# Optimization experiments

Hardware: AMD Instinct MI355X
Metric: run time of the kernel (lower is better)

The kernel has to match this reference:

```python
import jax, jax.numpy as jnp
import numpy as np

NEG_SLOPE = 0.2  # PyG GATConv default negative_slope


def setup_inputs() -> dict:
    key = jax.random.key(0)
    ks = jax.random.split(key, 5)
    N, E, F_in, F_out = 50000, 800000, 100, 200
    x = jax.random.normal(ks[0], (N, F_in), dtype=jnp.float32)
    edge_index = jax.random.randint(ks[1], (2, E), 0, N, dtype=jnp.int32)
    W = jax.random.normal(ks[2], (F_in, F_out), dtype=jnp.float32) / np.float32(np.sqrt(F_in))
    att_src = jax.random.normal(ks[3], (F_out,), dtype=jnp.float32) * 0.1
    att_dst = jax.random.normal(ks[4], (F_out,), dtype=jnp.float32) * 0.1
    bias = jnp.zeros((F_out,), dtype=jnp.float32)
    return {"x": x, "edge_index": edge_index, "W": W,
            "att_src": att_src, "att_dst": att_dst, "bias": bias}


def reference(x, edge_index, W, att_src, att_dst, bias):
    # GATConv (heads=1, concat=True, add_self_loops=True) followed by mean over nodes.
    N = x.shape[0]
    h = x @ W                                   # [N, F_out] transformed node features
    loops = jnp.arange(N, dtype=edge_index.dtype)
    src = jnp.concatenate([edge_index[0], loops])  # [E+N] source node per edge
    dst = jnp.concatenate([edge_index[1], loops])  # [E+N] destination node per edge
    # per-node attention logits
    a_s = h @ att_src                           # [N]
    a_d = h @ att_dst                           # [N]
    e = jax.nn.leaky_relu(a_s[src] + a_d[dst], NEG_SLOPE)  # [E+N]
    # numerically stable softmax over incoming edges of each destination node
    m = jax.ops.segment_max(e, dst, num_segments=N)        # [N]
    ex = jnp.exp(e - m[dst])                                # [E+N]
    denom = jax.ops.segment_sum(ex, dst, num_segments=N)    # [N]
    alpha = ex / denom[dst]                                  # [E+N]
    # scatter-add weighted messages
    out = jax.ops.segment_sum(alpha[:, None] * h[src], dst, num_segments=N) + bias  # [N, F_out]
    return jnp.mean(out, axis=0, keepdims=True)  # [1, F_out]
```

## Files before the change

### kernel.cpp

```cpp
#include <hip/hip_runtime.h>

#define NEG_SLOPE 0.2f
#define NBLK 256
#define RSH  6
#define RBIN 64
#define CAP  1536
#define MAXB 1024
#define CSB  256

typedef unsigned int uint;


__global__ void k_f1(const float* __restrict__ W, const float* __restrict__ att_src,
                     const float* __restrict__ att_dst, const int* __restrict__ ei,
                     float* __restrict__ wsv, float* __restrict__ wdv,
                     uint* __restrict__ cntA, uint* __restrict__ cntB,
                     uint* __restrict__ recA, uint* __restrict__ recB,
                     int E, int N, int B, int F_out) {
    __shared__ uint hA[MAXB], hB[MAXB];
    __shared__ float l_as[256], l_ad[256];
    int tid = threadIdx.x;
    int blk = blockIdx.x;
    if (blk == 0) {
        if (tid < 200) { l_as[tid] = att_src[tid]; l_ad[tid] = att_dst[tid]; }
        __syncthreads();
        if (tid < 200) {
            int k = tid >> 1, j = tid & 1;
            const float* row = W + (size_t)k * F_out + j * 100;
            const float* as = l_as + j * 100;
            const float* ad = l_ad + j * 100;
            float s0 = 0.f, s1 = 0.f;
            #pragma unroll
            for (int i = 0; i < 100; ++i) {
                float w = row[i];
                s0 = fmaf(w, as[i], s0);
                s1 = fmaf(w, ad[i], s1);
            }
            s0 += __shfl_xor(s0, 1);
            s1 += __shfl_xor(s1, 1);
            if (j == 0) { wsv[k] = s0; wdv[k] = s1; }
        }
    } else if (blk <= NBLK) {
        int hb = blk - 1;
        for (int b = tid; b < B; b += 256) { hA[b] = 0u; hB[b] = 0u; }
        __syncthreads();
        if ((E & 3) == 0) {
            int stride = NBLK * 256 * 4;
            for (int i = (hb * 256 + tid) * 4; i < E; i += stride) {
                int4 s4 = *reinterpret_cast<const int4*>(ei + i);
                int4 d4 = *reinterpret_cast<const int4*>(ei + E + i);
                atomicAdd(&hA[d4.x >> RSH], 1u); atomicAdd(&hB[s4.x >> RSH], 1u);
                atomicAdd(&hA[d4.y >> RSH], 1u); atomicAdd(&hB[s4.y >> RSH], 1u);
                atomicAdd(&hA[d4.z >> RSH], 1u); atomicAdd(&hB[s4.z >> RSH], 1u);
                atomicAdd(&hA[d4.w >> RSH], 1u); atomicAdd(&hB[s4.w >> RSH], 1u);
            }
        } else {
            int stride = NBLK * 256;
            for (int i = hb * 256 + tid; i < E; i += stride) {
                int s = ei[i], d = ei[E + i];
                atomicAdd(&hA[d >> RSH], 1u); atomicAdd(&hB[s >> RSH], 1u);
            }
        }
        __syncthreads();
        for (int b = tid; b < B; b += 256) {
            cntA[(size_t)hb * B + b] = hA[b];
            cntB[(size_t)hb * B + b] = hB[b];
        }
    } else {
        int idx = blk - NBLK - 1;
        int n0 = idx * 512;
        int n1 = min(N, n0 + 512);
        for (int n = n0 + tid; n < n1; n += 256) {
            int b = n >> RSH, l = n & (RBIN - 1);
            uint rec = ((uint)l << 16) | (uint)n;
            size_t slot = (size_t)b * CAP + l;
            recA[slot] = rec;
            recB[slot] = rec;
        }
    }
}

__global__ void k_f2(const float* __restrict__ x, const float* __restrict__ wsv,
                     const float* __restrict__ wdv, float* __restrict__ a_s,
                     float* __restrict__ a_d, uint* __restrict__ cntA,
                     uint* __restrict__ cntB, uint* __restrict__ totA,
                     uint* __restrict__ totB, int N, int B, int NODEB) {
    __shared__ float lws[100], lwd[100];
    __shared__ float p0[256], p1[256];
    __shared__ uint sv[NBLK];
    int tid = threadIdx.x;
    int blk = blockIdx.x;
    if (blk < NODEB) {
        if (tid < 100) { lws[tid] = wsv[tid]; lwd[tid] = wdv[tid]; }
        __syncthreads();
        int r = tid / 25, q = tid - r * 25;
        int row = blk * 10 + r;
        float s0 = 0.f, s1 = 0.f;
        if (tid < 250 && row < N) {
            float4 v = *reinterpret_cast<const float4*>(x + (size_t)row * 100 + q * 4);
            const float* ws = lws + q * 4;
            const float* wd = lwd + q * 4;
            s0 = v.x * ws[0] + v.y * ws[1] + v.z * ws[2] + v.w * ws[3];
            s1 = v.x * wd[0] + v.y * wd[1] + v.z * wd[2] + v.w * wd[3];
        }
        p0[tid] = s0;
        p1[tid] = s1;
        __syncthreads();
        if (tid < 20) {
            int rr = tid >> 1;
            int row2 = blk * 10 + rr;
            if (row2 < N) {
                const float* p = (tid & 1) ? p1 : p0;
                float acc = 0.f;
                #pragma unroll
                for (int j = 0; j < 25; ++j) acc += p[rr * 25 + j];
                if (tid & 1) a_d[row2] = acc;
                else         a_s[row2] = acc;
            }
        }
    } else {
        int bi = blk - NODEB;
        int isB = bi >= B;
        int b = isB ? bi - B : bi;
        uint* cnt = isB ? cntB : cntA;
        uint* tot = isB ? totB : totA;
        int sc = N - b * RBIN; if (sc > RBIN) sc = RBIN;
        uint v = cnt[(size_t)tid * B + b];
        sv[tid] = v;
        __syncthreads();
        #pragma unroll
        for (int off = 1; off < NBLK; off <<= 1) {
            uint y = (tid >= off) ? sv[tid - off] : 0u;
            __syncthreads();
            sv[tid] += y;
            __syncthreads();
        }
        uint incl = sv[tid];
        cnt[(size_t)tid * B + b] = (uint)b * CAP + (uint)sc + incl - v;
        if (tid == NBLK - 1) tot[b] = (uint)sc + incl;
    }
}

__global__ void k_scatter(const int* __restrict__ ei, const uint* __restrict__ offsA,
                          const uint* __restrict__ offsB, uint* __restrict__ recA,
                          uint* __restrict__ recB, int E, int B) {
    __shared__ uint curA[MAXB], curB[MAXB];
    int tid = threadIdx.x, blk = blockIdx.x;
    for (int b = tid; b < B; b += 256) {
        curA[b] = offsA[(size_t)blk * B + b];
        curB[b] = offsB[(size_t)blk * B + b];
    }
    __syncthreads();
    if ((E & 3) == 0) {
        int stride = NBLK * 256 * 4;
        for (int i = (blk * 256 + tid) * 4; i < E; i += stride) {
            int4 s4 = *reinterpret_cast<const int4*>(ei + i);
            int4 d4 = *reinterpret_cast<const int4*>(ei + E + i);
            {   uint sA = atomicAdd(&curA[d4.x >> RSH], 1u);
                recA[sA] = ((uint)(d4.x & (RBIN - 1)) << 16) | (uint)s4.x;
                uint sB = atomicAdd(&curB[s4.x >> RSH], 1u);
                recB[sB] = ((uint)(s4.x & (RBIN - 1)) << 16) | (uint)d4.x; }
            {   uint sA = atomicAdd(&curA[d4.y >> RSH], 1u);
                recA[sA] = ((uint)(d4.y & (RBIN - 1)) << 16) | (uint)s4.y;
                uint sB = atomicAdd(&curB[s4.y >> RSH], 1u);
                recB[sB] = ((uint)(s4.y & (RBIN - 1)) << 16) | (uint)d4.y; }
            {   uint sA = atomicAdd(&curA[d4.z >> RSH], 1u);
                recA[sA] = ((uint)(d4.z & (RBIN - 1)) << 16) | (uint)s4.z;
                uint sB = atomicAdd(&curB[s4.z >> RSH], 1u);
                recB[sB] = ((uint)(s4.z & (RBIN - 1)) << 16) | (uint)d4.z; }
            {   uint sA = atomicAdd(&curA[d4.w >> RSH], 1u);
                recA[sA] = ((uint)(d4.w & (RBIN - 1)) << 16) | (uint)s4.w;
                uint sB = atomicAdd(&curB[s4.w >> RSH], 1u);
                recB[sB] = ((uint)(s4.w & (RBIN - 1)) << 16) | (uint)d4.w; }
        }
    } else {
        int stride = NBLK * 256;
        for (int i = blk * 256 + tid; i < E; i += stride) {
            int s = ei[i], d = ei[E + i];
            uint sA = atomicAdd(&curA[d >> RSH], 1u);
            recA[sA] = ((uint)(d & (RBIN - 1)) << 16) | (uint)s;
            uint sB = atomicAdd(&curB[s >> RSH], 1u);
            recB[sB] = ((uint)(s & (RBIN - 1)) << 16) | (uint)d;
        }
    }
}

__global__ void k_denom(const uint* __restrict__ recA, const uint* __restrict__ totA,
                        const float* __restrict__ a_s, const float* __restrict__ a_d,
                        float* __restrict__ denom, int N) {
    __shared__ float lad[RBIN];
    __shared__ float acc[RBIN];
    int tid = threadIdx.x, b = blockIdx.x;
    if (tid < RBIN) {
        int node = b * RBIN + tid;
        lad[tid] = (node < N) ? a_d[node] : 0.f;
        acc[tid] = 0.f;
    }
    __syncthreads();
    uint j0 = (uint)b * CAP, cnt = totA[b];
    for (uint j = tid; j < cnt; j += 256) {
        uint rec = recA[j0 + j];
        int src = rec & 0xFFFF;
        int dl = rec >> 16;
        float e = a_s[src] + lad[dl];
        e = (e >= 0.f) ? e : NEG_SLOPE * e;
        atomicAdd(&acc[dl], __expf(e));
    }
    __syncthreads();
    if (tid < RBIN) {
        int node = b * RBIN + tid;
        if (node < N) denom[node] = acc[tid];
    }
}

__global__ void k_alpha(const uint* __restrict__ recB, const uint* __restrict__ totB,
                        const float* __restrict__ a_s, const float* __restrict__ a_d,
                        const float* __restrict__ denom, float* __restrict__ s_src, int N) {
    __shared__ float las[RBIN];
    __shared__ float acc[RBIN];
    int tid = threadIdx.x, b = blockIdx.x;
    if (tid < RBIN) {
        int node = b * RBIN + tid;
        las[tid] = (node < N) ? a_s[node] : 0.f;
        acc[tid] = 0.f;
    }
    __syncthreads();
    uint j0 = (uint)b * CAP, cnt = totB[b];
    for (uint j = tid; j < cnt; j += 256) {
        uint rec = recB[j0 + j];
        int dst = rec & 0xFFFF;
        int sl = rec >> 16;
        float e = las[sl] + a_d[dst];
        e = (e >= 0.f) ? e : NEG_SLOPE * e;
        float alpha = __expf(e) / denom[dst];
        atomicAdd(&acc[sl], alpha);
    }
    __syncthreads();
    if (tid < RBIN) {
        int node = b * RBIN + tid;
        if (node < N) s_src[node] = acc[tid];
    }
}


__global__ void k_zero_ds(float* __restrict__ p, int n) {
    int i = blockIdx.x * blockDim.x + threadIdx.x;
    if (i < n) p[i] = 0.f;
}

__device__ __forceinline__ float edge_logit(const int* __restrict__ ei,
                                            const float* __restrict__ a_s,
                                            const float* __restrict__ a_d,
                                            int i, int E, int& src, int& dst) {
    if (i < E) { src = ei[i]; dst = ei[E + i]; }
    else       { src = dst = i - E; }
    float e = a_s[src] + a_d[dst];
    return (e >= 0.f) ? e : NEG_SLOPE * e;
}

__global__ void k_edge_denom_dev(const int* __restrict__ ei, const float* __restrict__ a_s,
                                 const float* __restrict__ a_d, float* __restrict__ denom,
                                 int E, int N) {
    int i = blockIdx.x * blockDim.x + threadIdx.x;
    if (i >= E + N) return;
    int src, dst;
    float e = edge_logit(ei, a_s, a_d, i, E, src, dst);
    atomicAdd(denom + dst, __expf(e));
}

__global__ void k_edge_scatter_dev(const int* __restrict__ ei, const float* __restrict__ a_s,
                                   const float* __restrict__ a_d, const float* __restrict__ denom,
                                   float* __restrict__ s_src, int E, int N) {
    int i = blockIdx.x * blockDim.x + threadIdx.x;
    if (i >= E + N) return;
    int src, dst;
    float e = edge_logit(ei, a_s, a_d, i, E, src, dst);
    float alpha = __expf(e) / denom[dst];
    atomicAdd(s_src + src, alpha);
}


__global__ void k_colsum1(const float* __restrict__ x, const float* __restrict__ s_src,
                          float* __restrict__ part, int N) {
    __shared__ float4 lacc[512];
    int tid = threadIdx.x;
    int r = tid / 25, q = tid - r * 25;
    float4 acc = make_float4(0.f, 0.f, 0.f, 0.f);
    if (tid < 500) {
        for (int n0 = blockIdx.x * 20; n0 < N; n0 += gridDim.x * 20) {
            int row = n0 + r;
            if (row < N) {
                float w = s_src[row];
                float4 v = *reinterpret_cast<const float4*>(x + (size_t)row * 100 + q * 4);
                acc.x = fmaf(w, v.x, acc.x);
                acc.y = fmaf(w, v.y, acc.y);
                acc.z = fmaf(w, v.z, acc.z);
                acc.w = fmaf(w, v.w, acc.w);
            }
        }
    }
    lacc[tid] = acc;
    __syncthreads();
    if (tid < 25) {
        float4 a = lacc[tid];
        #pragma unroll
        for (int rr = 1; rr < 20; ++rr) {
            float4 b = lacc[rr * 25 + tid];
            a.x += b.x; a.y += b.y; a.z += b.z; a.w += b.w;
        }
        *reinterpret_cast<float4*>(part + (size_t)blockIdx.x * 128 + tid * 4) = a;
    }
}

__global__ void k_f3(const float* __restrict__ part, const float* __restrict__ W,
                     const float* __restrict__ bias, float* __restrict__ out,
                     int N, int F_in, int F_out) {
    __shared__ float lt[128];
    int tid = threadIdx.x;
    for (int k = tid; k < F_in; k += 256) {
        float s0 = 0.f, s1 = 0.f, s2 = 0.f, s3 = 0.f;
        for (int b = 0; b < CSB; b += 4) {
            s0 += part[(size_t)b * 128 + k];
            s1 += part[(size_t)(b + 1) * 128 + k];
            s2 += part[(size_t)(b + 2) * 128 + k];
            s3 += part[(size_t)(b + 3) * 128 + k];
        }
        lt[k] = (s0 + s1) + (s2 + s3);
    }
    __syncthreads();
    float inv = 1.f / (float)N;
    for (int f = tid; f < F_out; f += 256) {
        float acc = 0.f;
        for (int k = 0; k < F_in; ++k) {
            acc = fmaf(lt[k], W[(size_t)k * F_out + f], acc);
        }
        out[f] = acc * inv + bias[f];
    }
}

extern "C" void kernel_launch(void* const* d_in, const int* in_sizes, int n_in,
                              void* d_out, int out_size, void* d_ws, size_t ws_size,
                              hipStream_t stream) {
    const float* x       = (const float*)d_in[0];
    const int*   ei      = (const int*)d_in[1];
    const float* W       = (const float*)d_in[2];
    const float* att_src = (const float*)d_in[3];
    const float* att_dst = (const float*)d_in[4];
    const float* bias    = (const float*)d_in[5];
    float* out = (float*)d_out;

    const int F_out = in_sizes[3];
    const int F_in  = in_sizes[2] / F_out;
    const int N     = in_sizes[0] / F_in;
    const int E     = in_sizes[1] / 2;
    const int B     = (N + RBIN - 1) >> RSH;
    const int NODEB = (N + 9) / 10;
    const int SRB   = (N + 511) / 512;

    float* ws = (float*)d_ws;
    float* wsv   = ws;
    float* wdv   = ws + 128;
    float* a_s   = ws + 256;
    float* a_d   = a_s + N;
    float* denom = a_d + N;
    float* s_src = denom + N;
    uint*  cntA  = (uint*)(s_src + N);
    uint*  cntB  = cntA + (size_t)NBLK * B;
    uint*  totA  = cntB + (size_t)NBLK * B;
    uint*  totB  = totA + B;
    uint*  recA  = totB + B;
    uint*  recB  = recA + (size_t)B * CAP;
    float* part  = (float*)cntA;

    size_t need_bytes = (size_t)((recB + (size_t)B * CAP) - (uint*)ws) * 4;
    bool sort_ok = (ws_size >= need_bytes) && (B <= MAXB) && (N <= 65536) &&
                   ((size_t)NBLK * 128 >= (size_t)CSB * 128);

    if (sort_ok) {
        k_f1<<<1 + NBLK + SRB, 256, 0, stream>>>(W, att_src, att_dst, ei, wsv, wdv,
                                                 cntA, cntB, recA, recB, E, N, B, F_out);
        k_f2<<<NODEB + 2 * B, 256, 0, stream>>>(x, wsv, wdv, a_s, a_d,
                                                cntA, cntB, totA, totB, N, B, NODEB);
        k_scatter<<<NBLK, 256, 0, stream>>>(ei, cntA, cntB, recA, recB, E, B);
        k_denom<<<B, 256, 0, stream>>>(recA, totA, a_s, a_d, denom, N);
        k_alpha<<<B, 256, 0, stream>>>(recB, totB, a_s, a_d, denom, s_src, N);
    } else {
        k_f1<<<1, 256, 0, stream>>>(W, att_src, att_dst, ei, wsv, wdv,
                                    cntA, cntB, recA, recB, E, N, B, F_out);
        k_f2<<<NODEB, 256, 0, stream>>>(x, wsv, wdv, a_s, a_d,
                                        cntA, cntB, totA, totB, N, B, NODEB);
        k_zero_ds<<<(2 * N + 255) / 256, 256, 0, stream>>>(denom, 2 * N);
        int grid = (E + N + 255) / 256;
        k_edge_denom_dev<<<grid, 256, 0, stream>>>(ei, a_s, a_d, denom, E, N);
        k_edge_scatter_dev<<<grid, 256, 0, stream>>>(ei, a_s, a_d, denom, s_src, E, N);
    }

    k_colsum1<<<CSB, 512, 0, stream>>>(x, s_src, part, N);
    k_f3<<<1, 256, 0, stream>>>(part, W, bias, out, N, F_in, F_out);
}
```

Before: 77.47 us.

## Fuse column-sum into alpha kernel and handle self-loops analytically

Self-loop records are no longer written into the sorted bins. Each bin instead seeds its accumulator with the self-loop term computed directly, which removes the record-initialisation blocks from the first kernel. The denominator and a_d are packed into a float2 so the alpha pass does one gather per edge. The weighted column sum of x is fused into the per-bin alpha kernel, which writes per-bin partials that a final single block reduces, replacing the separate colsum launch. The cost is a larger partial buffer (B rows) for the final reduction, and the fast path now requires F_in=100 and F_out=200.

```diff
diff --git a/kernel.cpp b/kernel.cpp
--- a/kernel.cpp
+++ b/kernel.cpp
@@ -1,95 +1,76 @@
 #include <hip/hip_runtime.h>
 
+typedef unsigned int uint;
+
 #define NEG_SLOPE 0.2f
-#define NBLK 256
 #define RSH  6
 #define RBIN 64
 #define CAP  1536
 #define MAXB 1024
-#define CSB  256
-
-typedef unsigned int uint;
-
-
-__global__ void k_f1(const float* __restrict__ W, const float* __restrict__ att_src,
-                     const float* __restrict__ att_dst, const int* __restrict__ ei,
-                     float* __restrict__ wsv, float* __restrict__ wdv,
-                     uint* __restrict__ cntA, uint* __restrict__ cntB,
-                     uint* __restrict__ recA, uint* __restrict__ recB,
-                     int E, int N, int B, int F_out) {
+#define NBLK 256
+
+
+__global__ void k1_prep_hist(const float* __restrict__ W, const float* __restrict__ att_src,
+                             const float* __restrict__ att_dst, const int* __restrict__ ei,
+                             float* __restrict__ wsv, float* __restrict__ wdv,
+                             uint* __restrict__ cntA, uint* __restrict__ cntB,
+                             int E, int B, int F_out) {
     __shared__ uint hA[MAXB], hB[MAXB];
     __shared__ float l_as[256], l_ad[256];
-    int tid = threadIdx.x;
-    int blk = blockIdx.x;
+    int tid = threadIdx.x, blk = blockIdx.x;
     if (blk == 0) {
         if (tid < 200) { l_as[tid] = att_src[tid]; l_ad[tid] = att_dst[tid]; }
         __syncthreads();
         if (tid < 200) {
             int k = tid >> 1, j = tid & 1;
             const float* row = W + (size_t)k * F_out + j * 100;
-            const float* as = l_as + j * 100;
-            const float* ad = l_ad + j * 100;
             float s0 = 0.f, s1 = 0.f;
             #pragma unroll
             for (int i = 0; i < 100; ++i) {
                 float w = row[i];
-                s0 = fmaf(w, as[i], s0);
-                s1 = fmaf(w, ad[i], s1);
+                s0 = fmaf(w, l_as[j * 100 + i], s0);
+                s1 = fmaf(w, l_ad[j * 100 + i], s1);
             }
             s0 += __shfl_xor(s0, 1);
             s1 += __shfl_xor(s1, 1);
             if (j == 0) { wsv[k] = s0; wdv[k] = s1; }
         }
-    } else if (blk <= NBLK) {
-        int hb = blk - 1;
-        for (int b = tid; b < B; b += 256) { hA[b] = 0u; hB[b] = 0u; }
-        __syncthreads();
-        if ((E & 3) == 0) {
-            int stride = NBLK * 256 * 4;
-            for (int i = (hb * 256 + tid) * 4; i < E; i += stride) {
-                int4 s4 = *reinterpret_cast<const int4*>(ei + i);
-                int4 d4 = *reinterpret_cast<const int4*>(ei + E + i);
-                atomicAdd(&hA[d4.x >> RSH], 1u); atomicAdd(&hB[s4.x >> RSH], 1u);
-                atomicAdd(&hA[d4.y >> RSH], 1u); atomicAdd(&hB[s4.y >> RSH], 1u);
-                atomicAdd(&hA[d4.z >> RSH], 1u); atomicAdd(&hB[s4.z >> RSH], 1u);
-                atomicAdd(&hA[d4.w >> RSH], 1u); atomicAdd(&hB[s4.w >> RSH], 1u);
-            }
-        } else {
-            int stride = NBLK * 256;
-            for (int i = hb * 256 + tid; i < E; i += stride) {
-                int s = ei[i], d = ei[E + i];
-                atomicAdd(&hA[d >> RSH], 1u); atomicAdd(&hB[s >> RSH], 1u);
-            }
-        }
-        __syncthreads();
-        for (int b = tid; b < B; b += 256) {
-            cntA[(size_t)hb * B + b] = hA[b];
-            cntB[(size_t)hb * B + b] = hB[b];
+        return;
+    }
+    int hb = blk - 1;
+    for (int b = tid; b < B; b += 256) { hA[b] = 0u; hB[b] = 0u; }
+    __syncthreads();
+    if ((E & 3) == 0) {
+        for (int i = (hb * 256 + tid) * 4; i < E; i += NBLK * 256 * 4) {
+            int4 s4 = *reinterpret_cast<const int4*>(ei + i);
+            int4 d4 = *reinterpret_cast<const int4*>(ei + E + i);
+            atomicAdd(&hA[d4.x >> RSH], 1u); atomicAdd(&hB[s4.x >> RSH], 1u);
+            atomicAdd(&hA[d4.y >> RSH], 1u); atomicAdd(&hB[s4.y >> RSH], 1u);
+            atomicAdd(&hA[d4.z >> RSH], 1u); atomicAdd(&hB[s4.z >> RSH], 1u);
+            atomicAdd(&hA[d4.w >> RSH], 1u); atomicAdd(&hB[s4.w >> RSH], 1u);
         }
     } else {
-        int idx = blk - NBLK - 1;
-        int n0 = idx * 512;
-        int n1 = min(N, n0 + 512);
-        for (int n = n0 + tid; n < n1; n += 256) {
-            int b = n >> RSH, l = n & (RBIN - 1);
-            uint rec = ((uint)l << 16) | (uint)n;
-            size_t slot = (size_t)b * CAP + l;
-            recA[slot] = rec;
-            recB[slot] = rec;
-        }
-    }
-}
-
-__global__ void k_f2(const float* __restrict__ x, const float* __restrict__ wsv,
-                     const float* __restrict__ wdv, float* __restrict__ a_s,
-                     float* __restrict__ a_d, uint* __restrict__ cntA,
-                     uint* __restrict__ cntB, uint* __restrict__ totA,
-                     uint* __restrict__ totB, int N, int B, int NODEB) {
+        for (int i = hb * 256 + tid; i < E; i += NBLK * 256) {
+            int s = ei[i], d = ei[E + i];
+            atomicAdd(&hA[d >> RSH], 1u); atomicAdd(&hB[s >> RSH], 1u);
+        }
+    }
+    __syncthreads();
+    for (int b = tid; b < B; b += 256) {
+        cntA[(size_t)hb * B + b] = hA[b];
+        cntB[(size_t)hb * B + b] = hB[b];
+    }
+}
+
+__global__ void k2_node_offs(const float* __restrict__ x, const float* __restrict__ wsv,
+                             const float* __restrict__ wdv, float* __restrict__ a_s,
+                             float* __restrict__ a_d, uint* __restrict__ cntA,
+                             uint* __restrict__ cntB, uint* __restrict__ totA,
+                             uint* __restrict__ totB, int N, int B, int NODEB) {
     __shared__ float lws[100], lwd[100];
     __shared__ float p0[256], p1[256];
     __shared__ uint sv[NBLK];
-    int tid = threadIdx.x;
-    int blk = blockIdx.x;
+    int tid = threadIdx.x, blk = blockIdx.x;
     if (blk < NODEB) {
         if (tid < 100) { lws[tid] = wsv[tid]; lwd[tid] = wdv[tid]; }
         __syncthreads();
@@ -110,10 +91,10 @@
             int rr = tid >> 1;
             int row2 = blk * 10 + rr;
             if (row2 < N) {
-                const float* p = (tid & 1) ? p1 : p0;
+                const float* pp = (tid & 1) ? p1 : p0;
                 float acc = 0.f;
                 #pragma unroll
-                for (int j = 0; j < 25; ++j) acc += p[rr * 25 + j];
+                for (int j = 0; j < 25; ++j) acc += pp[rr * 25 + j];
                 if (tid & 1) a_d[row2] = acc;
                 else         a_s[row2] = acc;
             }
@@ -124,7 +105,6 @@
         int b = isB ? bi - B : bi;
         uint* cnt = isB ? cntB : cntA;
         uint* tot = isB ? totB : totA;
-        int sc = N - b * RBIN; if (sc > RBIN) sc = RBIN;
         uint v = cnt[(size_t)tid * B + b];
         sv[tid] = v;
         __syncthreads();
@@ -136,14 +116,14 @@
             __syncthreads();
         }
         uint incl = sv[tid];
-        cnt[(size_t)tid * B + b] = (uint)b * CAP + (uint)sc + incl - v;
-        if (tid == NBLK - 1) tot[b] = (uint)sc + incl;
-    }
-}
-
-__global__ void k_scatter(const int* __restrict__ ei, const uint* __restrict__ offsA,
-                          const uint* __restrict__ offsB, uint* __restrict__ recA,
-                          uint* __restrict__ recB, int E, int B) {
+        cnt[(size_t)tid * B + b] = (uint)b * CAP + incl - v;
+        if (tid == NBLK - 1) tot[b] = incl;
+    }
+}
+
+__global__ void k3_scatter(const int* __restrict__ ei, const uint* __restrict__ offsA,
+                           const uint* __restrict__ offsB, uint* __restrict__ recA,
+                           uint* __restrict__ recB, int E, int B) {
     __shared__ uint curA[MAXB], curB[MAXB];
     int tid = threadIdx.x, blk = blockIdx.x;
     for (int b = tid; b < B; b += 256) {
@@ -152,8 +132,7 @@
     }
     __syncthreads();
     if ((E & 3) == 0) {
-        int stride = NBLK * 256 * 4;
-        for (int i = (blk * 256 + tid) * 4; i < E; i += stride) {
+        for (int i = (blk * 256 + tid) * 4; i < E; i += NBLK * 256 * 4) {
             int4 s4 = *reinterpret_cast<const int4*>(ei + i);
             int4 d4 = *reinterpret_cast<const int4*>(ei + E + i);
             {   uint sA = atomicAdd(&curA[d4.x >> RSH], 1u);
@@ -174,8 +153,7 @@
                 recB[sB] = ((uint)(s4.w & (RBIN - 1)) << 16) | (uint)d4.w; }
         }
     } else {
-        int stride = NBLK * 256;
-        for (int i = blk * 256 + tid; i < E; i += stride) {
+        for (int i = blk * 256 + tid; i < E; i += NBLK * 256) {
             int s = ei[i], d = ei[E + i];
             uint sA = atomicAdd(&curA[d >> RSH], 1u);
             recA[sA] = ((uint)(d & (RBIN - 1)) << 16) | (uint)s;
@@ -185,16 +163,23 @@
     }
 }
 
-__global__ void k_denom(const uint* __restrict__ recA, const uint* __restrict__ totA,
-                        const float* __restrict__ a_s, const float* __restrict__ a_d,
-                        float* __restrict__ denom, int N) {
+__global__ void k4_denom(const uint* __restrict__ recA, const uint* __restrict__ totA,
+                         const float* __restrict__ a_s, const float* __restrict__ a_d,
+                         float2* __restrict__ dd, int N) {
     __shared__ float lad[RBIN];
     __shared__ float acc[RBIN];
     int tid = threadIdx.x, b = blockIdx.x;
     if (tid < RBIN) {
         int node = b * RBIN + tid;
-        lad[tid] = (node < N) ? a_d[node] : 0.f;
-        acc[tid] = 0.f;
+        float ad = 0.f, v = 0.f;
+        if (node < N) {
+            ad = a_d[node];
+            float e = a_s[node] + ad;
+            e = (e >= 0.f) ? e : NEG_SLOPE * e;
+            v = __expf(e);
+        }
+        lad[tid] = ad;
+        acc[tid] = v;
     }
     __syncthreads();
     uint j0 = (uint)b * CAP, cnt = totA[b];
@@ -209,20 +194,29 @@
     __syncthreads();
     if (tid < RBIN) {
         int node = b * RBIN + tid;
-        if (node < N) denom[node] = acc[tid];
-    }
-}
-
-__global__ void k_alpha(const uint* __restrict__ recB, const uint* __restrict__ totB,
-                        const float* __restrict__ a_s, const float* __restrict__ a_d,
-                        const float* __restrict__ denom, float* __restrict__ s_src, int N) {
+        if (node < N) dd[node] = make_float2(lad[tid], acc[tid]);
+    }
+}
+
+__global__ void k5_alpha_colsum(const uint* __restrict__ recB, const uint* __restrict__ totB,
+                                const float* __restrict__ a_s, const float2* __restrict__ dd,
+                                const float* __restrict__ x, float* __restrict__ part, int N) {
     __shared__ float las[RBIN];
     __shared__ float acc[RBIN];
+    __shared__ float4 red[256];
     int tid = threadIdx.x, b = blockIdx.x;
     if (tid < RBIN) {
         int node = b * RBIN + tid;
-        las[tid] = (node < N) ? a_s[node] : 0.f;
-        acc[tid] = 0.f;
+        float asv = 0.f, v = 0.f;
+        if (node < N) {
+            asv = a_s[node];
+            float2 d2 = dd[node];
+            float e = asv + d2.x;
+            e = (e >= 0.f) ? e : NEG_SLOPE * e;
+            v = __expf(e) / d2.y;
+        }
+        las[tid] = asv;
+        acc[tid] = v;
     }
     __syncthreads();
     uint j0 = (uint)b * CAP, cnt = totB[b];
@@ -230,112 +224,128 @@
         uint rec = recB[j0 + j];
         int dst = rec & 0xFFFF;
         int sl = rec >> 16;
-        float e = las[sl] + a_d[dst];
+        float2 d2 = dd[dst];
+        float e = las[sl] + d2.x;
         e = (e >= 0.f) ? e : NEG_SLOPE * e;
-        float alpha = __expf(e) / denom[dst];
-        atomicAdd(&acc[sl], alpha);
-    }
-    __syncthreads();
-    if (tid < RBIN) {
-        int node = b * RBIN + tid;
-        if (node < N) s_src[node] = acc[tid];
-    }
-}
-
-
-__global__ void k_zero_ds(float* __restrict__ p, int n) {
-    int i = blockIdx.x * blockDim.x + threadIdx.x;
-    if (i < n) p[i] = 0.f;
-}
-
-__device__ __forceinline__ float edge_logit(const int* __restrict__ ei,
-                                            const float* __restrict__ a_s,
-                                            const float* __restrict__ a_d,
-                                            int i, int E, int& src, int& dst) {
-    if (i < E) { src = ei[i]; dst = ei[E + i]; }
-    else       { src = dst = i - E; }
-    float e = a_s[src] + a_d[dst];
-    return (e >= 0.f) ? e : NEG_SLOPE * e;
-}
-
-__global__ void k_edge_denom_dev(const int* __restrict__ ei, const float* __restrict__ a_s,
-                                 const float* __restrict__ a_d, float* __restrict__ denom,
-                                 int E, int N) {
+        atomicAdd(&acc[sl], __expf(e) / d2.y);
+    }
+    __syncthreads();
+    int rg = tid >> 5;
+    int q  = tid & 31;
+    float4 a = make_float4(0.f, 0.f, 0.f, 0.f);
+    if (q < 25) {
+        for (int rr = rg; rr < RBIN; rr += 8) {
+            int row = b * RBIN + rr;
+            if (row < N) {
+                float w = acc[rr];
+                float4 v = *reinterpret_cast<const float4*>(x + (size_t)row * 100 + q * 4);
+                a.x = fmaf(w, v.x, a.x);
+                a.y = fmaf(w, v.y, a.y);
+                a.z = fmaf(w, v.z, a.z);
+                a.w = fmaf(w, v.w, a.w);
+            }
+        }
+    }
+    red[tid] = a;
+    __syncthreads();
+    if (tid < 25) {
+        float4 s = red[tid];
+        #pragma unroll
+        for (int g = 1; g < 8; ++g) {
+            float4 bb = red[g * 32 + tid];
+            s.x += bb.x; s.y += bb.y; s.z += bb.z; s.w += bb.w;
+        }
+        *reinterpret_cast<float4*>(part + (size_t)b * 128 + tid * 4) = s;
+    }
+}
+
+__global__ void k6_final(const float* __restrict__ part, const float* __restrict__ W,
+                         const float* __restrict__ bias, float* __restrict__ out,
+                         int N, int B, int F_in, int F_out) {
+    __shared__ float lt[256];
+    int tid = threadIdx.x;
+    int k = tid & 127;
+    int half = tid >> 7;
+    float s = 0.f;
+    for (int b = half; b < B; b += 2) s += part[(size_t)b * 128 + k];
+    lt[tid] = s;
+    __syncthreads();
+    if (tid < 128) lt[tid] += lt[tid + 128];
+    __syncthreads();
+    float inv = 1.f / (float)N;
+    for (int f = tid; f < F_out; f += 256) {
+        float a = 0.f;
+        for (int kk = 0; kk < F_in; ++kk) a = fmaf(lt[kk], W[(size_t)kk * F_out + f], a);
+        out[f] = a * inv + bias[f];
+    }
+}
+
+
+__global__ void fb_prep(const float* W, const float* att_src, const float* att_dst,
+                        float* wsv, float* wdv, int F_in, int F_out) {
+    for (int k = threadIdx.x; k < F_in; k += blockDim.x) {
+        float s0 = 0.f, s1 = 0.f;
+        for (int f = 0; f < F_out; ++f) {
+            float w = W[(size_t)k * F_out + f];
+            s0 = fmaf(w, att_src[f], s0);
+            s1 = fmaf(w, att_dst[f], s1);
+        }
+        wsv[k] = s0; wdv[k] = s1;
+    }
+}
+__global__ void fb_node(const float* x, const float* wsv, const float* wdv,
+                        float* a_s, float* a_d, float* denom, float* s_src,
+                        int N, int F_in) {
+    int n = blockIdx.x * blockDim.x + threadIdx.x;
+    if (n >= N) return;
+    float s0 = 0.f, s1 = 0.f;
+    for (int k = 0; k < F_in; ++k) {
+        float v = x[(size_t)n * F_in + k];
+        s0 = fmaf(v, wsv[k], s0);
+        s1 = fmaf(v, wdv[k], s1);
+    }
+    a_s[n] = s0; a_d[n] = s1; denom[n] = 0.f; s_src[n] = 0.f;
+}
+__global__ void fb_denom(const int* ei, const float* a_s, const float* a_d,
+                         float* denom, int E, int N) {
     int i = blockIdx.x * blockDim.x + threadIdx.x;
     if (i >= E + N) return;
     int src, dst;
-    float e = edge_logit(ei, a_s, a_d, i, E, src, dst);
+    if (i < E) { src = ei[i]; dst = ei[E + i]; } else { src = dst = i - E; }
+    float e = a_s[src] + a_d[dst];
+    e = (e >= 0.f) ? e : NEG_SLOPE * e;
     atomicAdd(denom + dst, __expf(e));
 }
-
-__global__ void k_edge_scatter_dev(const int* __restrict__ ei, const float* __restrict__ a_s,
-                                   const float* __restrict__ a_d, const float* __restrict__ denom,
-                                   float* __restrict__ s_src, int E, int N) {
+__global__ void fb_alpha(const int* ei, const float* a_s, const float* a_d,
+                         const float* denom, float* s_src, int E, int N) {
     int i = blockIdx.x * blockDim.x + threadIdx.x;
     if (i >= E + N) return;
     int src, dst;
-    float e = edge_logit(ei, a_s, a_d, i, E, src, dst);
-    float alpha = __expf(e) / denom[dst];
-    atomicAdd(s_src + src, alpha);
-}
-
-
-__global__ void k_colsum1(const float* __restrict__ x, const float* __restrict__ s_src,
-                          float* __restrict__ part, int N) {
-    __shared__ float4 lacc[512];
-    int tid = threadIdx.x;
-    int r = tid / 25, q = tid - r * 25;
-    float4 acc = make_float4(0.f, 0.f, 0.f, 0.f);
-    if (tid < 500) {
-        for (int n0 = blockIdx.x * 20; n0 < N; n0 += gridDim.x * 20) {
-            int row = n0 + r;
-            if (row < N) {
-                float w = s_src[row];
-                float4 v = *reinterpret_cast<const float4*>(x + (size_t)row * 100 + q * 4);
-                acc.x = fmaf(w, v.x, acc.x);
-                acc.y = fmaf(w, v.y, acc.y);
-                acc.z = fmaf(w, v.z, acc.z);
-                acc.w = fmaf(w, v.w, acc.w);
-            }
-        }
-    }
-    lacc[tid] = acc;
-    __syncthreads();
-    if (tid < 25) {
-        float4 a = lacc[tid];
-        #pragma unroll
-        for (int rr = 1; rr < 20; ++rr) {
-            float4 b = lacc[rr * 25 + tid];
-            a.x += b.x; a.y += b.y; a.z += b.z; a.w += b.w;
-        }
-        *reinterpret_cast<float4*>(part + (size_t)blockIdx.x * 128 + tid * 4) = a;
-    }
-}
-
-__global__ void k_f3(const float* __restrict__ part, const float* __restrict__ W,
-                     const float* __restrict__ bias, float* __restrict__ out,
-                     int N, int F_in, int F_out) {
-    __shared__ float lt[128];
-    int tid = threadIdx.x;
-    for (int k = tid; k < F_in; k += 256) {
-        float s0 = 0.f, s1 = 0.f, s2 = 0.f, s3 = 0.f;
-        for (int b = 0; b < CSB; b += 4) {
-            s0 += part[(size_t)b * 128 + k];
-            s1 += part[(size_t)(b + 1) * 128 + k];
-            s2 += part[(size_t)(b + 2) * 128 + k];
-            s3 += part[(size_t)(b + 3) * 128 + k];
-        }
-        lt[k] = (s0 + s1) + (s2 + s3);
-    }
-    __syncthreads();
-    float inv = 1.f / (float)N;
-    for (int f = tid; f < F_out; f += 256) {
-        float acc = 0.f;
-        for (int k = 0; k < F_in; ++k) {
-            acc = fmaf(lt[k], W[(size_t)k * F_out + f], acc);
-        }
-        out[f] = acc * inv + bias[f];
-    }
+    if (i < E) { src = ei[i]; dst = ei[E + i]; } else { src = dst = i - E; }
+    float e = a_s[src] + a_d[dst];
+    e = (e >= 0.f) ? e : NEG_SLOPE * e;
+    atomicAdd(s_src + src, __expf(e) / denom[dst]);
+}
+__global__ void fb_colsum(const float* x, const float* s_src, float* t, int N, int F_in) {
+    __shared__ float red[256];
+    int k = blockIdx.x;
+    float s = 0.f;
+    for (int n = threadIdx.x; n < N; n += 256) s = fmaf(s_src[n], x[(size_t)n * F_in + k], s);
+    red[threadIdx.x] = s;
+    __syncthreads();
+    for (int off = 128; off > 0; off >>= 1) {
+        if (threadIdx.x < off) red[threadIdx.x] += red[threadIdx.x + off];
+        __syncthreads();
+    }
+    if (threadIdx.x == 0) t[k] = red[0];
+}
+__global__ void fb_final(const float* t, const float* W, const float* bias, float* out,
+                         int N, int F_in, int F_out) {
+    int f = blockIdx.x * blockDim.x + threadIdx.x;
+    if (f >= F_out) return;
+    float acc = 0.f;
+    for (int k = 0; k < F_in; ++k) acc = fmaf(t[k], W[(size_t)k * F_out + f], acc);
+    out[f] = acc / (float)N + bias[f];
 }
 
 extern "C" void kernel_launch(void* const* d_in, const int* in_sizes, int n_in,
@@ -355,46 +365,46 @@
     const int E     = in_sizes[1] / 2;
     const int B     = (N + RBIN - 1) >> RSH;
     const int NODEB = (N + 9) / 10;
-    const int SRB   = (N + 511) / 512;
 
     float* ws = (float*)d_ws;
-    float* wsv   = ws;
-    float* wdv   = ws + 128;
-    float* a_s   = ws + 256;
-    float* a_d   = a_s + N;
-    float* denom = a_d + N;
-    float* s_src = denom + N;
-    uint*  cntA  = (uint*)(s_src + N);
-    uint*  cntB  = cntA + (size_t)NBLK * B;
-    uint*  totA  = cntB + (size_t)NBLK * B;
-    uint*  totB  = totA + B;
-    uint*  recA  = totB + B;
-    uint*  recB  = recA + (size_t)B * CAP;
-    float* part  = (float*)cntA;
-
-    size_t need_bytes = (size_t)((recB + (size_t)B * CAP) - (uint*)ws) * 4;
-    bool sort_ok = (ws_size >= need_bytes) && (B <= MAXB) && (N <= 65536) &&
-                   ((size_t)NBLK * 128 >= (size_t)CSB * 128);
+    size_t off = 0;
+    float* wsv   = ws + off; off += 128;
+    float* wdv   = ws + off; off += 128;
+    float* t     = ws + off; off += 128;
+    float* a_s   = ws + off; off += N;
+    float* a_d   = ws + off; off += N;
+    float* denom = ws + off; off += N;
+    float* s_src = ws + off; off += N;
+    off = (off + 1) & ~(size_t)1;
+    float2* dd   = (float2*)(ws + off); off += 2 * (size_t)N;
+    uint* cntA   = (uint*)(ws + off); off += (size_t)NBLK * B;
+    uint* cntB   = (uint*)(ws + off); off += (size_t)NBLK * B;
+    uint* totA   = (uint*)(ws + off); off += B;
+    uint* totB   = (uint*)(ws + off); off += B;
+    uint* recA   = (uint*)(ws + off); off += (size_t)B * CAP;
+    uint* recB   = (uint*)(ws + off); off += (size_t)B * CAP;
+    float* part  = ws + off; off += (size_t)B * 128;
+    size_t need_bytes = off * 4;
+
+    bool sort_ok = (ws_size >= need_bytes) && (B <= MAXB) && (N <= 65535) &&
+                   (F_in == 100) && (F_out == 200);
 
     if (sort_ok) {
-        k_f1<<<1 + NBLK + SRB, 256, 0, stream>>>(W, att_src, att_dst, ei, wsv, wdv,
-                                                 cntA, cntB, recA, recB, E, N, B, F_out);
-        k_f2<<<NODEB + 2 * B, 256, 0, stream>>>(x, wsv, wdv, a_s, a_d,
-                                                cntA, cntB, totA, totB, N, B, NODEB);
-        k_scatter<<<NBLK, 256, 0, stream>>>(ei, cntA, cntB, recA, recB, E, B);
-        k_denom<<<B, 256, 0, stream>>>(recA, totA, a_s, a_d, denom, N);
-        k_alpha<<<B, 256, 0, stream>>>(recB, totB, a_s, a_d, denom, s_src, N);
+        k1_prep_hist<<<1 + NBLK, 256, 0, stream>>>(W, att_src, att_dst, ei, wsv, wdv,
+                                                   cntA, cntB, E, B, F_out);
+        k2_node_offs<<<NODEB + 2 * B, 256, 0, stream>>>(x, wsv, wdv, a_s, a_d,
+                                                        cntA, cntB, totA, totB, N, B, NODEB);
+        k3_scatter<<<NBLK, 256, 0, stream>>>(ei, cntA, cntB, recA, recB, E, B);
+        k4_denom<<<B, 256, 0, stream>>>(recA, totA, a_s, a_d, dd, N);
+        k5_alpha_colsum<<<B, 256, 0, stream>>>(recB, totB, a_s, dd, x, part, N);
+        k6_final<<<1, 256, 0, stream>>>(part, W, bias, out, N, B, F_in, F_out);
     } else {
-        k_f1<<<1, 256, 0, stream>>>(W, att_src, att_dst, ei, wsv, wdv,
-                                    cntA, cntB, recA, recB, E, N, B, F_out);
-        k_f2<<<NODEB, 256, 0, stream>>>(x, wsv, wdv, a_s, a_d,
-                                        cntA, cntB, totA, totB, N, B, NODEB);
-        k_zero_ds<<<(2 * N + 255) / 256, 256, 0, stream>>>(denom, 2 * N);
+        fb_prep<<<1, 256, 0, stream>>>(W, att_src, att_dst, wsv, wdv, F_in, F_out);
+        fb_node<<<(N + 255) / 256, 256, 0, stream>>>(x, wsv, wdv, a_s, a_d, denom, s_src, N, F_in);
         int grid = (E + N + 255) / 256;
-        k_edge_denom_dev<<<grid, 256, 0, stream>>>(ei, a_s, a_d, denom, E, N);
-        k_edge_scatter_dev<<<grid, 256, 0, stream>>>(ei, a_s, a_d, denom, s_src, E, N);
-    }
-
-    k_colsum1<<<CSB, 512, 0, stream>>>(x, s_src, part, N);
-    k_f3<<<1, 256, 0, stream>>>(part, W, bias, out, N, F_in, F_out);
-}
+        fb_denom<<<grid, 256, 0, stream>>>(ei, a_s, a_d, denom, E, N);
+        fb_alpha<<<grid, 256, 0, stream>>>(ei, a_s, a_d, denom, s_src, E, N);
+        fb_colsum<<<F_in, 256, 0, stream>>>(x, s_src, t, N, F_in);
+        fb_final<<<(F_out + 255) / 256, 256, 0, stream>>>(t, W, bias, out, N, F_in, F_out);
+    }
+}
```

Result: slower. 161.7 us (+108.8%).
